# Optimization experiments

Hardware: AMD Instinct MI355X
Metric: run time of the kernel (lower is better)

The kernel has to match this reference:

```python
import jax, jax.numpy as jnp
import numpy as np

B, S, HID = 2, 2048, 2048
NH, NKV, HD = 16, 2, 128
N_REP = NH // NKV
SCALE = HD ** -0.5
NEG = -1e9


def rotate_half(x):
    x1, x2 = x[..., : HD // 2], x[..., HD // 2 :]
    return jnp.concatenate((-x2, x1), axis=-1)


def setup_inputs() -> dict:
    key = jax.random.key(0)
    ks = jax.random.split(key, 8)
    hidden_states = jax.random.normal(ks[0], (B, S, HID), jnp.float32)
    # RoPE tables (theta=10000), shape [B, S, HD]
    inv_freq = 1.0 / (10000.0 ** (np.arange(0, HD, 2, dtype=np.float32) / HD))
    pos = np.arange(S, dtype=np.float32)
    freqs = np.outer(pos, inv_freq)  # [S, HD/2]
    emb = np.concatenate([freqs, freqs], axis=-1)  # [S, HD]
    cos = jnp.broadcast_to(jnp.asarray(np.cos(emb)), (B, S, HD))
    sin = jnp.broadcast_to(jnp.asarray(np.sin(emb)), (B, S, HD))
    # additive causal mask [B, 1, S, S]
    causal = jnp.where(jnp.tril(jnp.ones((S, S), bool)), 0.0, NEG).astype(jnp.float32)
    attention_mask = jnp.broadcast_to(causal[None, None], (B, 1, S, S))
    sc = 0.02
    return {
        "hidden_states": hidden_states,
        "cos": cos,
        "sin": sin,
        "attention_mask": attention_mask,
        "Wq": jax.random.normal(ks[1], (NH * HD, HID), jnp.float32) * sc,
        "bq": jax.random.normal(ks[2], (NH * HD,), jnp.float32) * sc,
        "Wk": jax.random.normal(ks[3], (NKV * HD, HID), jnp.float32) * sc,
        "bk": jax.random.normal(ks[4], (NKV * HD,), jnp.float32) * sc,
        "Wv": jax.random.normal(ks[5], (NKV * HD, HID), jnp.float32) * sc,
        "bv": jax.random.normal(ks[6], (NKV * HD,), jnp.float32) * sc,
        "Wo": jax.random.normal(ks[7], (HID, NH * HD), jnp.float32) * sc,
    }


def reference(hidden_states, cos, sin, attention_mask, Wq, bq, Wk, bk, Wv, bv, Wo):
    b, s, _ = hidden_states.shape
    # QKV projections -> [B, H, S, D]
    q = (hidden_states @ Wq.T + bq).reshape(b, s, NH, HD).transpose(0, 2, 1, 3)
    k = (hidden_states @ Wk.T + bk).reshape(b, s, NKV, HD).transpose(0, 2, 1, 3)
    v = (hidden_states @ Wv.T + bv).reshape(b, s, NKV, HD).transpose(0, 2, 1, 3)
    # RoPE (cos/sin unsqueezed at head dim)
    c, si = cos[:, None], sin[:, None]
    q = q * c + rotate_half(q) * si
    k = k * c + rotate_half(k) * si
    # GQA: repeat kv heads
    k = jnp.repeat(k, N_REP, axis=1)
    v = jnp.repeat(v, N_REP, axis=1)
    scores = jnp.einsum("bhqd,bhkd->bhqk", q, k) * SCALE
    scores = scores + attention_mask[:, :, :, :s]
    attn_weights = jax.nn.softmax(scores.astype(jnp.float32), axis=-1).astype(q.dtype)
    attn_out = jnp.einsum("bhqk,bhkd->bhqd", attn_weights, v)
    attn_out = attn_out.transpose(0, 2, 1, 3).reshape(b, s, NH * HD)
    out = attn_out @ Wo.T
    return out, attn_weights
```

## Files before the change

### kernel.cpp

```cpp
#include <hip/hip_runtime.h>
#include <hip/hip_bf16.h>
#include <cstdint>

constexpr int Bb  = 2;
constexpr int Ss  = 2048;
constexpr int HID = 2048;
constexpr int NH  = 16;
constexpr int NKV = 2;
constexpr int HD  = 128;
constexpr int Mrows = Bb * Ss;
constexpr float SCALE = 0.08838834764831845f;

typedef __bf16 bf16_t;
typedef __attribute__((ext_vector_type(8))) __bf16 bf16x8;
typedef __attribute__((ext_vector_type(4))) __bf16 bf16x4;
typedef __attribute__((ext_vector_type(4))) float f32x4;

static __device__ __forceinline__ f32x4 mfma16(bf16x8 a, bf16x8 b, f32x4 c) {
  return __builtin_amdgcn_mfma_f32_16x16x32_bf16(a, b, c, 0, 0, 0);
}

static __device__ __forceinline__ void stage_async(bf16_t* lds, const bf16_t* src,
                                                   int ld, int tid) {
#pragma unroll
  for (int it = 0; it < 2; ++it) {
    int c = tid + it * 256;
    int row = c >> 2, kc = c & 3;
    __builtin_amdgcn_global_load_lds(
        (const __attribute__((address_space(1))) void*)(src + (size_t)row * ld + kc * 8),
        (__attribute__((address_space(3))) void*)(lds + c * 8), 16, 0, 0);
  }
}

template <int IM, int JM>
static __device__ __forceinline__ void wave_mma(const bf16_t* As, const bf16_t* Bs,
                                                f32x4 (&acc)[IM][JM], int wm, int wn,
                                                int lane) {
  const int q = lane >> 4, r = lane & 15;
  bf16x8 a[IM], b[JM];
#pragma unroll
  for (int i = 0; i < IM; ++i)
    a[i] = *(const bf16x8*)(As + (wm + i * 16 + r) * 32 + q * 8);
#pragma unroll
  for (int j = 0; j < JM; ++j)
    b[j] = *(const bf16x8*)(Bs + (wn + j * 16 + r) * 32 + q * 8);
#pragma unroll
  for (int i = 0; i < IM; ++i)
#pragma unroll
    for (int j = 0; j < JM; ++j)
      acc[i][j] = mfma16(a[i], b[j], acc[i][j]);
}

__global__ void cvt_bf16_kernel(const float* __restrict__ in, bf16_t* __restrict__ out) {
  size_t i = ((size_t)blockIdx.x * 256 + threadIdx.x) * 8;
  float4 a = *(const float4*)(in + i);
  float4 b = *(const float4*)(in + i + 4);
  bf16x8 v;
  v[0] = (__bf16)a.x; v[1] = (__bf16)a.y; v[2] = (__bf16)a.z; v[3] = (__bf16)a.w;
  v[4] = (__bf16)b.x; v[5] = (__bf16)b.y; v[6] = (__bf16)b.z; v[7] = (__bf16)b.w;
  *(bf16x8*)(out + i) = v;
}

__global__ void zero_kernel(float* __restrict__ p) {
  p[(size_t)blockIdx.x * 256 + threadIdx.x] = 0.0f;
}

__global__ __launch_bounds__(256) void proj_kernel(
    const bf16_t* __restrict__ A, const bf16_t* __restrict__ Bt,
    const float* __restrict__ bq, const float* __restrict__ bk,
    const float* __restrict__ bv, const float* __restrict__ cosb,
    const float* __restrict__ sinb, bf16_t* __restrict__ q_bf,
    bf16_t* __restrict__ k_bf, bf16_t* __restrict__ v_t) {
  __shared__ __align__(16) bf16_t As[128 * 32];
  __shared__ __align__(16) bf16_t Bs[128 * 32];
  const int tid = threadIdx.x;
  const int bx = blockIdx.x;
  const int m0 = blockIdx.y * 128, n0 = bx * 128;
  const int lane = tid & 63, w = tid >> 6;
  const int wm = w * 32;
  const int q = lane >> 4, r = lane & 15;
  f32x4 acc[2][8];
#pragma unroll
  for (int i = 0; i < 2; ++i)
#pragma unroll
    for (int j = 0; j < 8; ++j) acc[i][j] = (f32x4){0.f, 0.f, 0.f, 0.f};
  const bf16_t* Ap = A + (size_t)m0 * HID;
  const bf16_t* Bp = Bt + (size_t)n0 * HID;
  for (int k0 = 0; k0 < HID; k0 += 32) {
    stage_async(As, Ap + k0, HID, tid);
    stage_async(Bs, Bp + k0, HID, tid);
    __syncthreads();
    wave_mma<2, 8>(As, Bs, acc, wm, 0, lane);
    __syncthreads();
  }
  const float* bias_base;
  int mode;
  int hh;
  if (bx < 16) { mode = 0; hh = bx; bias_base = bq + n0; }
  else if (bx < 18) { mode = 1; hh = bx - 16; bias_base = bk + (bx - 16) * 128; }
  else { mode = 2; hh = bx - 18; bias_base = bv + (bx - 18) * 128; }
  float bias_j[8];
#pragma unroll
  for (int j = 0; j < 8; ++j) bias_j[j] = bias_base[j * 16 + r];
  float e[2][8][4];
#pragma unroll
  for (int i = 0; i < 2; ++i)
#pragma unroll
    for (int j = 0; j < 8; ++j)
#pragma unroll
      for (int t = 0; t < 4; ++t) e[i][j][t] = acc[i][j][t] + bias_j[j];

  if (mode == 2) {
#pragma unroll
    for (int i = 0; i < 2; ++i) {
      int s_base = m0 + wm + i * 16 + q * 4;
      int bI = s_base >> 11, s = s_base & 2047;
#pragma unroll
      for (int j = 0; j < 8; ++j) {
        int d = j * 16 + r;
        bf16x4 pk;
#pragma unroll
        for (int t = 0; t < 4; ++t) pk[t] = (__bf16)e[i][j][t];
        *(bf16x4*)(v_t + ((size_t)(bI * NKV + hh) * HD + d) * Ss + s) = pk;
      }
    }
  } else {
    bf16_t* dst_base = (mode == 0) ? q_bf : k_bf;
    const int nhv = (mode == 0) ? NH : NKV;
#pragma unroll
    for (int i = 0; i < 2; ++i) {
#pragma unroll
      for (int t = 0; t < 4; ++t) {
        int s_glob = m0 + wm + i * 16 + q * 4 + t;
        int bI = s_glob >> 11, s = s_glob & 2047;
        const float* cp = cosb + ((size_t)bI * Ss + s) * HD;
        const float* sp = sinb + ((size_t)bI * Ss + s) * HD;
        bf16_t* dst = dst_base + ((size_t)(bI * nhv + hh) * Ss + s) * HD;
#pragma unroll
        for (int j = 0; j < 8; ++j) {
          int d = j * 16 + r;
          float c = cp[d], sn = sp[d];
          float p = e[i][j ^ 4][t];
          float o = e[i][j][t] * c + ((j < 4) ? -p : p) * sn;
          dst[d] = (__bf16)o;
        }
      }
    }
  }
}

__global__ __launch_bounds__(256) void qs_kernel(const bf16_t* __restrict__ qb,
                                                 const bf16_t* __restrict__ kb,
                                                 float* __restrict__ rowsum) {
  const int tj = blockIdx.x, ti = blockIdx.y;
  if (tj > ti) return;
  const int bh = blockIdx.z;
  const int b = bh >> 4, h = bh & 15, kv = h >> 3;
  __shared__ __align__(16) bf16_t As[128 * 32];
  __shared__ __align__(16) bf16_t Bs[128 * 32];
  __shared__ float rs[128];
  const int tid = threadIdx.x;
  if (tid < 128) rs[tid] = 0.0f;
  const int lane = tid & 63, w = tid >> 6;
  const int wm = (w >> 1) * 64, wn = (w & 1) * 64;
  const int q = lane >> 4, r = lane & 15;
  f32x4 acc[4][4];
#pragma unroll
  for (int i = 0; i < 4; ++i)
#pragma unroll
    for (int j = 0; j < 4; ++j) acc[i][j] = (f32x4){0.f, 0.f, 0.f, 0.f};
  const bf16_t* Ap = qb + (size_t)bh * Ss * HD + (size_t)ti * 128 * HD;
  const bf16_t* Bp = kb + (size_t)(b * NKV + kv) * Ss * HD + (size_t)tj * 128 * HD;
#pragma unroll
  for (int k0 = 0; k0 < HD; k0 += 32) {
    stage_async(As, Ap + k0, HD, tid);
    stage_async(Bs, Bp + k0, HD, tid);
    __syncthreads();
    wave_mma<4, 4>(As, Bs, acc, wm, wn, lane);
    __syncthreads();
  }
  const bool diag = (ti == tj);
  float rp[4][4];
#pragma unroll
  for (int i = 0; i < 4; ++i)
#pragma unroll
    for (int t = 0; t < 4; ++t) rp[i][t] = 0.0f;
#pragma unroll
  for (int i = 0; i < 4; ++i) {
#pragma unroll
    for (int t = 0; t < 4; ++t) {
      int row_l = wm + i * 16 + q * 4 + t;
#pragma unroll
      for (int j = 0; j < 4; ++j) {
        int col_l = wn + j * 16 + r;
        float ev = (diag && col_l > row_l) ? 0.0f : __expf(acc[i][j][t] * SCALE);
        rp[i][t] += ev;
      }
    }
  }
#pragma unroll
  for (int off = 1; off < 16; off <<= 1)
#pragma unroll
    for (int i = 0; i < 4; ++i)
#pragma unroll
      for (int t = 0; t < 4; ++t) rp[i][t] += __shfl_xor(rp[i][t], off, 64);
  if (r == 0) {
#pragma unroll
    for (int i = 0; i < 4; ++i)
#pragma unroll
      for (int t = 0; t < 4; ++t)
        atomicAdd(&rs[wm + i * 16 + q * 4 + t], rp[i][t]);
  }
  __syncthreads();
  if (tid < 128)
    atomicAdd(rowsum + (size_t)bh * Ss + (size_t)ti * 128 + tid, rs[tid]);
}

__global__ __launch_bounds__(256, 2) void spv_kernel(
    const bf16_t* __restrict__ qb, const bf16_t* __restrict__ kb,
    const bf16_t* __restrict__ vt, const float* __restrict__ rowsum,
    float* __restrict__ attn, bf16_t* __restrict__ ao) {
  const int mt = blockIdx.y;
  const int bh = blockIdx.z;
  const int b = bh >> 4, h = bh & 15, kv = h >> 3;
  __shared__ __align__(16) bf16_t Ks[4][128 * 32];
  __shared__ __align__(16) bf16_t Ps[128 * 136];
  __shared__ float inv_s[128];
  const int tid = threadIdx.x;
  if (tid < 128)
    inv_s[tid] = 1.0f / rowsum[(size_t)bh * Ss + (size_t)mt * 128 + tid];
  const int lane = tid & 63, w = tid >> 6;
  const int wm = (w >> 1) * 64, wn = (w & 1) * 64;
  const int q = lane >> 4, r = lane & 15;

  const bf16_t* Qp = qb + (size_t)bh * Ss * HD + (size_t)mt * 128 * HD;
#pragma unroll
  for (int s = 0; s < 4; ++s) stage_async(Ks[s], Qp + s * 32, HD, tid);
  __syncthreads();
  bf16x8 aq[4][4];
#pragma unroll
  for (int s = 0; s < 4; ++s)
#pragma unroll
    for (int i = 0; i < 4; ++i)
      aq[s][i] = *(const bf16x8*)(Ks[s] + (wm + i * 16 + r) * 32 + q * 8);
  float inv_my[4][4];
#pragma unroll
  for (int i = 0; i < 4; ++i)
#pragma unroll
    for (int t = 0; t < 4; ++t)
      inv_my[i][t] = inv_s[wm + i * 16 + q * 4 + t];
  __syncthreads();

  const bf16_t* Kp = kb + (size_t)(b * NKV + kv) * Ss * HD;
  const bf16_t* Vp = vt + (size_t)(b * NKV + kv) * HD * Ss;
  float* Arow = attn + ((size_t)bh * Ss + (size_t)mt * 128) * Ss;

  f32x4 acc2[4][4];
#pragma unroll
  for (int i = 0; i < 4; ++i)
#pragma unroll
    for (int j = 0; j < 4; ++j) acc2[i][j] = (f32x4){0.f, 0.f, 0.f, 0.f};

  for (int kt = 0; kt <= mt; ++kt) {
#pragma unroll
    for (int s = 0; s < 4; ++s)
      stage_async(Ks[s], Kp + (size_t)kt * 128 * HD + s * 32, HD, tid);
    __syncthreads();
    f32x4 acc[4][4];
#pragma unroll
    for (int i = 0; i < 4; ++i)
#pragma unroll
      for (int j = 0; j < 4; ++j) acc[i][j] = (f32x4){0.f, 0.f, 0.f, 0.f};
#pragma unroll
    for (int s = 0; s < 4; ++s) {
      bf16x8 bfr[4];
#pragma unroll
      for (int j = 0; j < 4; ++j)
        bfr[j] = *(const bf16x8*)(Ks[s] + (wn + j * 16 + r) * 32 + q * 8);
#pragma unroll
      for (int i = 0; i < 4; ++i)
#pragma unroll
        for (int j = 0; j < 4; ++j)
          acc[i][j] = mfma16(aq[s][i], bfr[j], acc[i][j]);
    }
    const bool diag = (kt == mt);
#pragma unroll
    for (int i = 0; i < 4; ++i) {
#pragma unroll
      for (int t = 0; t < 4; ++t) {
        int row_l = wm + i * 16 + q * 4 + t;
        float inv = inv_my[i][t];
        float* orow = Arow + (size_t)row_l * Ss + kt * 128;
#pragma unroll
        for (int j = 0; j < 4; ++j) {
          int col_l = wn + j * 16 + r;
          float ev = (diag && col_l > row_l)
                         ? 0.0f
                         : __expf(acc[i][j][t] * SCALE) * inv;
          orow[col_l] = ev;
          Ps[row_l * 136 + col_l] = (__bf16)ev;
        }
      }
    }
    __syncthreads();
#pragma unroll
    for (int s = 0; s < 4; ++s)
      stage_async(Ks[s], Vp + kt * 128 + s * 32, Ss, tid);
    __syncthreads();
#pragma unroll
    for (int s = 0; s < 4; ++s) {
      bf16x8 ap[4], bv4[4];
#pragma unroll
      for (int i = 0; i < 4; ++i)
        ap[i] = *(const bf16x8*)(Ps + (wm + i * 16 + r) * 136 + s * 32 + q * 8);
#pragma unroll
      for (int j = 0; j < 4; ++j)
        bv4[j] = *(const bf16x8*)(Ks[s] + (wn + j * 16 + r) * 32 + q * 8);
#pragma unroll
      for (int i = 0; i < 4; ++i)
#pragma unroll
        for (int j = 0; j < 4; ++j)
          acc2[i][j] = mfma16(ap[i], bv4[j], acc2[i][j]);
    }
    __syncthreads();
  }

  const int kmax = (mt + 1) * 128;
  const int width = Ss - kmax;
  if (width > 0) {
    const float4 z4 = {0.f, 0.f, 0.f, 0.f};
    for (int rr = 0; rr < 128; ++rr) {
      float* zp = Arow + (size_t)rr * Ss + kmax;
      for (int cc = tid * 4; cc < width; cc += 1024) *(float4*)(zp + cc) = z4;
    }
  }
#pragma unroll
  for (int i = 0; i < 4; ++i) {
#pragma unroll
    for (int t = 0; t < 4; ++t) {
      int row = mt * 128 + wm + i * 16 + q * 4 + t;
#pragma unroll
      for (int j = 0; j < 4; ++j) {
        int col = wn + j * 16 + r;
        ao[(((size_t)b * Ss + row) * NH + h) * HD + col] = (__bf16)acc2[i][j][t];
      }
    }
  }
}

__global__ __launch_bounds__(256) void out_kernel(const bf16_t* __restrict__ A,
                                                  const bf16_t* __restrict__ Bt,
                                                  float* __restrict__ outp) {
  __shared__ __align__(16) bf16_t As[128 * 32];
  __shared__ __align__(16) bf16_t Bs[128 * 32];
  const int tid = threadIdx.x;
  const int m0 = blockIdx.y * 128, n0 = blockIdx.x * 128;
  const int lane = tid & 63, w = tid >> 6;
  const int wm = (w >> 1) * 64, wn = (w & 1) * 64;
  const int q = lane >> 4, r = lane & 15;
  f32x4 acc[4][4];
#pragma unroll
  for (int i = 0; i < 4; ++i)
#pragma unroll
    for (int j = 0; j < 4; ++j) acc[i][j] = (f32x4){0.f, 0.f, 0.f, 0.f};
  const bf16_t* Ap = A + (size_t)m0 * HID;
  const bf16_t* Bp = Bt + (size_t)n0 * HID;
  for (int k0 = 0; k0 < HID; k0 += 32) {
    stage_async(As, Ap + k0, HID, tid);
    stage_async(Bs, Bp + k0, HID, tid);
    __syncthreads();
    wave_mma<4, 4>(As, Bs, acc, wm, wn, lane);
    __syncthreads();
  }
#pragma unroll
  for (int i = 0; i < 4; ++i) {
#pragma unroll
    for (int t = 0; t < 4; ++t) {
      int row = m0 + wm + i * 16 + q * 4 + t;
#pragma unroll
      for (int j = 0; j < 4; ++j) {
        int col = n0 + wn + j * 16 + r;
        outp[(size_t)row * HID + col] = acc[i][j][t];
      }
    }
  }
}

extern "C" void kernel_launch(void* const* d_in, const int* in_sizes, int n_in,
                              void* d_out, int out_size, void* d_ws, size_t ws_size,
                              hipStream_t stream) {
  const float* hs   = (const float*)d_in[0];
  const float* cosb = (const float*)d_in[1];
  const float* sinb = (const float*)d_in[2];
  const float* Wq = (const float*)d_in[4];
  const float* bq = (const float*)d_in[5];
  const float* Wk = (const float*)d_in[6];
  const float* bk = (const float*)d_in[7];
  const float* Wv = (const float*)d_in[8];
  const float* bv = (const float*)d_in[9];
  const float* Wo = (const float*)d_in[10];

  float* out  = (float*)d_out;
  float* attn = out + (size_t)Bb * Ss * HID;

  char* wsp = (char*)d_ws;
  auto alloc = [&](size_t bytes) -> char* {
    char* p = wsp;
    wsp += (bytes + 255) & ~(size_t)255;
    return p;
  };
  bf16_t* hs_bf = (bf16_t*)alloc((size_t)Mrows * HID * 2);
  bf16_t* wqkv  = (bf16_t*)alloc((size_t)2560 * HID * 2);
  bf16_t* wo_bf = (bf16_t*)alloc((size_t)HID * NH * HD * 2);
  bf16_t* q_bf  = (bf16_t*)alloc((size_t)Mrows * NH * HD * 2);
  bf16_t* k_bf  = (bf16_t*)alloc((size_t)Bb * NKV * Ss * HD * 2);
  bf16_t* v_t   = (bf16_t*)alloc((size_t)Bb * NKV * Ss * HD * 2);
  bf16_t* ao_bf = (bf16_t*)alloc((size_t)Mrows * NH * HD * 2);
  float*  rs_ws = (float*)alloc((size_t)Bb * NH * Ss * 4);

  zero_kernel<<<(Bb * NH * Ss) / 256, 256, 0, stream>>>(rs_ws);

  cvt_bf16_kernel<<<(Mrows * HID) / 2048, 256, 0, stream>>>(hs, hs_bf);
  cvt_bf16_kernel<<<(NH * HD * HID) / 2048, 256, 0, stream>>>(Wq, wqkv);
  cvt_bf16_kernel<<<(NKV * HD * HID) / 2048, 256, 0, stream>>>(Wk, wqkv + (size_t)2048 * HID);
  cvt_bf16_kernel<<<(NKV * HD * HID) / 2048, 256, 0, stream>>>(Wv, wqkv + (size_t)2304 * HID);
  cvt_bf16_kernel<<<(HID * NH * HD) / 2048, 256, 0, stream>>>(Wo, wo_bf);

  proj_kernel<<<dim3(20, 32), 256, 0, stream>>>(hs_bf, wqkv, bq, bk, bv, cosb, sinb,
                                                q_bf, k_bf, v_t);

  qs_kernel<<<dim3(16, 16, Bb * NH), 256, 0, stream>>>(q_bf, k_bf, rs_ws);

  spv_kernel<<<dim3(1, 16, Bb * NH), 256, 0, stream>>>(q_bf, k_bf, v_t, rs_ws,
                                                       attn, ao_bf);

  out_kernel<<<dim3(16, 32), 256, 0, stream>>>(ao_bf, wo_bf, out);

  (void)in_sizes; (void)n_in; (void)out_size; (void)ws_size;
}
```

Before: 1.004 ms.

## Fuse row-sum pass into attention kernel with reordered tile schedule and prefetch

Removes the separate zero and row-sum kernels. The attention kernel now makes two passes over K tiles: the first accumulates exp row sums in LDS, and the second normalises, writes the probabilities and runs P·V. The grid is flattened so that each bh processes its light and heavy query tiles in a balanced order. K/V tile loads are issued early so they overlap the exp work, and the attention-weight stores are moved after the PV mma. The cost is that QK^T is computed twice inside one kernel, in exchange for dropping two launches, the global atomics and the rowsum round trip.

```diff
diff --git a/kernel.cpp b/kernel.cpp
--- a/kernel.cpp
+++ b/kernel.cpp
@@ -59,10 +59,6 @@
   v[0] = (__bf16)a.x; v[1] = (__bf16)a.y; v[2] = (__bf16)a.z; v[3] = (__bf16)a.w;
   v[4] = (__bf16)b.x; v[5] = (__bf16)b.y; v[6] = (__bf16)b.z; v[7] = (__bf16)b.w;
   *(bf16x8*)(out + i) = v;
-}
-
-__global__ void zero_kernel(float* __restrict__ p) {
-  p[(size_t)blockIdx.x * 256 + threadIdx.x] = 0.0f;
 }
 
 __global__ __launch_bounds__(256) void proj_kernel(
@@ -149,89 +145,25 @@
   }
 }
 
-__global__ __launch_bounds__(256) void qs_kernel(const bf16_t* __restrict__ qb,
-                                                 const bf16_t* __restrict__ kb,
-                                                 float* __restrict__ rowsum) {
-  const int tj = blockIdx.x, ti = blockIdx.y;
-  if (tj > ti) return;
-  const int bh = blockIdx.z;
+__global__ __launch_bounds__(256, 2) void spv_kernel(
+    const bf16_t* __restrict__ qb, const bf16_t* __restrict__ kb,
+    const bf16_t* __restrict__ vt, float* __restrict__ attn,
+    bf16_t* __restrict__ ao) {
+  const int bid = blockIdx.x;
+  const int slot = bid >> 8, p = bid & 255;
+  const int bh = p >> 3;
+  const int m3 = p & 7;
+  const int mt = slot ? (15 - m3) : m3;
   const int b = bh >> 4, h = bh & 15, kv = h >> 3;
-  __shared__ __align__(16) bf16_t As[128 * 32];
-  __shared__ __align__(16) bf16_t Bs[128 * 32];
+
+  __shared__ __align__(16) bf16_t Ks[4][128 * 32];
+  __shared__ __align__(16) bf16_t Ps[128 * 136];
   __shared__ float rs[128];
   const int tid = threadIdx.x;
   if (tid < 128) rs[tid] = 0.0f;
   const int lane = tid & 63, w = tid >> 6;
   const int wm = (w >> 1) * 64, wn = (w & 1) * 64;
   const int q = lane >> 4, r = lane & 15;
-  f32x4 acc[4][4];
-#pragma unroll
-  for (int i = 0; i < 4; ++i)
-#pragma unroll
-    for (int j = 0; j < 4; ++j) acc[i][j] = (f32x4){0.f, 0.f, 0.f, 0.f};
-  const bf16_t* Ap = qb + (size_t)bh * Ss * HD + (size_t)ti * 128 * HD;
-  const bf16_t* Bp = kb + (size_t)(b * NKV + kv) * Ss * HD + (size_t)tj * 128 * HD;
-#pragma unroll
-  for (int k0 = 0; k0 < HD; k0 += 32) {
-    stage_async(As, Ap + k0, HD, tid);
-    stage_async(Bs, Bp + k0, HD, tid);
-    __syncthreads();
-    wave_mma<4, 4>(As, Bs, acc, wm, wn, lane);
-    __syncthreads();
-  }
-  const bool diag = (ti == tj);
-  float rp[4][4];
-#pragma unroll
-  for (int i = 0; i < 4; ++i)
-#pragma unroll
-    for (int t = 0; t < 4; ++t) rp[i][t] = 0.0f;
-#pragma unroll
-  for (int i = 0; i < 4; ++i) {
-#pragma unroll
-    for (int t = 0; t < 4; ++t) {
-      int row_l = wm + i * 16 + q * 4 + t;
-#pragma unroll
-      for (int j = 0; j < 4; ++j) {
-        int col_l = wn + j * 16 + r;
-        float ev = (diag && col_l > row_l) ? 0.0f : __expf(acc[i][j][t] * SCALE);
-        rp[i][t] += ev;
-      }
-    }
-  }
-#pragma unroll
-  for (int off = 1; off < 16; off <<= 1)
-#pragma unroll
-    for (int i = 0; i < 4; ++i)
-#pragma unroll
-      for (int t = 0; t < 4; ++t) rp[i][t] += __shfl_xor(rp[i][t], off, 64);
-  if (r == 0) {
-#pragma unroll
-    for (int i = 0; i < 4; ++i)
-#pragma unroll
-      for (int t = 0; t < 4; ++t)
-        atomicAdd(&rs[wm + i * 16 + q * 4 + t], rp[i][t]);
-  }
-  __syncthreads();
-  if (tid < 128)
-    atomicAdd(rowsum + (size_t)bh * Ss + (size_t)ti * 128 + tid, rs[tid]);
-}
-
-__global__ __launch_bounds__(256, 2) void spv_kernel(
-    const bf16_t* __restrict__ qb, const bf16_t* __restrict__ kb,
-    const bf16_t* __restrict__ vt, const float* __restrict__ rowsum,
-    float* __restrict__ attn, bf16_t* __restrict__ ao) {
-  const int mt = blockIdx.y;
-  const int bh = blockIdx.z;
-  const int b = bh >> 4, h = bh & 15, kv = h >> 3;
-  __shared__ __align__(16) bf16_t Ks[4][128 * 32];
-  __shared__ __align__(16) bf16_t Ps[128 * 136];
-  __shared__ float inv_s[128];
-  const int tid = threadIdx.x;
-  if (tid < 128)
-    inv_s[tid] = 1.0f / rowsum[(size_t)bh * Ss + (size_t)mt * 128 + tid];
-  const int lane = tid & 63, w = tid >> 6;
-  const int wm = (w >> 1) * 64, wn = (w & 1) * 64;
-  const int q = lane >> 4, r = lane & 15;
 
   const bf16_t* Qp = qb + (size_t)bh * Ss * HD + (size_t)mt * 128 * HD;
 #pragma unroll
@@ -243,28 +175,20 @@
 #pragma unroll
     for (int i = 0; i < 4; ++i)
       aq[s][i] = *(const bf16x8*)(Ks[s] + (wm + i * 16 + r) * 32 + q * 8);
-  float inv_my[4][4];
-#pragma unroll
-  for (int i = 0; i < 4; ++i)
-#pragma unroll
-    for (int t = 0; t < 4; ++t)
-      inv_my[i][t] = inv_s[wm + i * 16 + q * 4 + t];
   __syncthreads();
 
   const bf16_t* Kp = kb + (size_t)(b * NKV + kv) * Ss * HD;
   const bf16_t* Vp = vt + (size_t)(b * NKV + kv) * HD * Ss;
   float* Arow = attn + ((size_t)bh * Ss + (size_t)mt * 128) * Ss;
 
-  f32x4 acc2[4][4];
+  float rp[4][4];
 #pragma unroll
   for (int i = 0; i < 4; ++i)
 #pragma unroll
-    for (int j = 0; j < 4; ++j) acc2[i][j] = (f32x4){0.f, 0.f, 0.f, 0.f};
-
+    for (int t = 0; t < 4; ++t) rp[i][t] = 0.0f;
+#pragma unroll
+  for (int s = 0; s < 4; ++s) stage_async(Ks[s], Kp + s * 32, HD, tid);
   for (int kt = 0; kt <= mt; ++kt) {
-#pragma unroll
-    for (int s = 0; s < 4; ++s)
-      stage_async(Ks[s], Kp + (size_t)kt * 128 * HD + s * 32, HD, tid);
     __syncthreads();
     f32x4 acc[4][4];
 #pragma unroll
@@ -283,6 +207,78 @@
         for (int j = 0; j < 4; ++j)
           acc[i][j] = mfma16(aq[s][i], bfr[j], acc[i][j]);
     }
+    __syncthreads();
+    if (kt < mt) {
+#pragma unroll
+      for (int s = 0; s < 4; ++s)
+        stage_async(Ks[s], Kp + (size_t)(kt + 1) * 128 * HD + s * 32, HD, tid);
+    }
+    const bool diag = (kt == mt);
+#pragma unroll
+    for (int i = 0; i < 4; ++i) {
+#pragma unroll
+      for (int t = 0; t < 4; ++t) {
+        int row_l = wm + i * 16 + q * 4 + t;
+#pragma unroll
+        for (int j = 0; j < 4; ++j) {
+          int col_l = wn + j * 16 + r;
+          float ev = (diag && col_l > row_l) ? 0.0f : __expf(acc[i][j][t] * SCALE);
+          rp[i][t] += ev;
+        }
+      }
+    }
+  }
+#pragma unroll
+  for (int off = 1; off < 16; off <<= 1)
+#pragma unroll
+    for (int i = 0; i < 4; ++i)
+#pragma unroll
+      for (int t = 0; t < 4; ++t) rp[i][t] += __shfl_xor(rp[i][t], off, 64);
+  if (r == 0) {
+#pragma unroll
+    for (int i = 0; i < 4; ++i)
+#pragma unroll
+      for (int t = 0; t < 4; ++t)
+        atomicAdd(&rs[wm + i * 16 + q * 4 + t], rp[i][t]);
+  }
+#pragma unroll
+  for (int s = 0; s < 4; ++s) stage_async(Ks[s], Kp + s * 32, HD, tid);
+  __syncthreads();
+  float inv_my[4][4];
+#pragma unroll
+  for (int i = 0; i < 4; ++i)
+#pragma unroll
+    for (int t = 0; t < 4; ++t)
+      inv_my[i][t] = 1.0f / rs[wm + i * 16 + q * 4 + t];
+
+  f32x4 acc2[4][4];
+#pragma unroll
+  for (int i = 0; i < 4; ++i)
+#pragma unroll
+    for (int j = 0; j < 4; ++j) acc2[i][j] = (f32x4){0.f, 0.f, 0.f, 0.f};
+
+  for (int kt = 0; kt <= mt; ++kt) {
+    f32x4 acc[4][4];
+#pragma unroll
+    for (int i = 0; i < 4; ++i)
+#pragma unroll
+      for (int j = 0; j < 4; ++j) acc[i][j] = (f32x4){0.f, 0.f, 0.f, 0.f};
+#pragma unroll
+    for (int s = 0; s < 4; ++s) {
+      bf16x8 bfr[4];
+#pragma unroll
+      for (int j = 0; j < 4; ++j)
+        bfr[j] = *(const bf16x8*)(Ks[s] + (wn + j * 16 + r) * 32 + q * 8);
+#pragma unroll
+      for (int i = 0; i < 4; ++i)
+#pragma unroll
+        for (int j = 0; j < 4; ++j)
+          acc[i][j] = mfma16(aq[s][i], bfr[j], acc[i][j]);
+    }
+    __syncthreads();
+#pragma unroll
+    for (int s = 0; s < 4; ++s)
+      stage_async(Ks[s], Vp + kt * 128 + s * 32, Ss, tid);
     const bool diag = (kt == mt);
 #pragma unroll
     for (int i = 0; i < 4; ++i) {
@@ -290,24 +286,19 @@
       for (int t = 0; t < 4; ++t) {
         int row_l = wm + i * 16 + q * 4 + t;
         float inv = inv_my[i][t];
-        float* orow = Arow + (size_t)row_l * Ss + kt * 128;
 #pragma unroll
         for (int j = 0; j < 4; ++j) {
           int col_l = wn + j * 16 + r;
           float ev = (diag && col_l > row_l)
                          ? 0.0f
                          : __expf(acc[i][j][t] * SCALE) * inv;
-          orow[col_l] = ev;
+          acc[i][j][t] = ev;
           Ps[row_l * 136 + col_l] = (__bf16)ev;
         }
       }
     }
     __syncthreads();
 #pragma unroll
-    for (int s = 0; s < 4; ++s)
-      stage_async(Ks[s], Vp + kt * 128 + s * 32, Ss, tid);
-    __syncthreads();
-#pragma unroll
     for (int s = 0; s < 4; ++s) {
       bf16x8 ap[4], bv4[4];
 #pragma unroll
@@ -323,6 +314,22 @@
           acc2[i][j] = mfma16(ap[i], bv4[j], acc2[i][j]);
     }
     __syncthreads();
+    if (kt < mt) {
+#pragma unroll
+      for (int s = 0; s < 4; ++s)
+        stage_async(Ks[s], Kp + (size_t)(kt + 1) * 128 * HD + s * 32, HD, tid);
+    }
+#pragma unroll
+    for (int i = 0; i < 4; ++i) {
+#pragma unroll
+      for (int t = 0; t < 4; ++t) {
+        int row_l = wm + i * 16 + q * 4 + t;
+        float* orow = Arow + (size_t)row_l * Ss + kt * 128;
+#pragma unroll
+        for (int j = 0; j < 4; ++j) orow[wn + j * 16 + r] = acc[i][j][t];
+      }
+    }
+    if (kt < mt) __syncthreads();
   }
 
   const int kmax = (mt + 1) * 128;
@@ -416,9 +423,6 @@
   bf16_t* k_bf  = (bf16_t*)alloc((size_t)Bb * NKV * Ss * HD * 2);
   bf16_t* v_t   = (bf16_t*)alloc((size_t)Bb * NKV * Ss * HD * 2);
   bf16_t* ao_bf = (bf16_t*)alloc((size_t)Mrows * NH * HD * 2);
-  float*  rs_ws = (float*)alloc((size_t)Bb * NH * Ss * 4);
-
-  zero_kernel<<<(Bb * NH * Ss) / 256, 256, 0, stream>>>(rs_ws);
 
   cvt_bf16_kernel<<<(Mrows * HID) / 2048, 256, 0, stream>>>(hs, hs_bf);
   cvt_bf16_kernel<<<(NH * HD * HID) / 2048, 256, 0, stream>>>(Wq, wqkv);
@@ -429,10 +433,7 @@
   proj_kernel<<<dim3(20, 32), 256, 0, stream>>>(hs_bf, wqkv, bq, bk, bv, cosb, sinb,
                                                 q_bf, k_bf, v_t);
 
-  qs_kernel<<<dim3(16, 16, Bb * NH), 256, 0, stream>>>(q_bf, k_bf, rs_ws);
-
-  spv_kernel<<<dim3(1, 16, Bb * NH), 256, 0, stream>>>(q_bf, k_bf, v_t, rs_ws,
-                                                       attn, ao_bf);
+  spv_kernel<<<dim3(512), 256, 0, stream>>>(q_bf, k_bf, v_t, attn, ao_bf);
 
   out_kernel<<<dim3(16, 32), 256, 0, stream>>>(ao_bf, wo_bf, out);
 
```

Result: faster. 929.3 us (-7.4%).
